# Optimization experiments

Hardware: AMD Instinct MI355X
Metric: run time of the kernel (lower is better)

The kernel has to match this reference:

```python
import jax, jax.numpy as jnp
import numpy as np

N_NODES = 50000
N_EDGES = 1600000
N_GRAPHS = 64
IN_DIM = 128
HID = 128
N_CLASSES = 10


def setup_inputs() -> dict:
    key = jax.random.key(0)
    ks = jax.random.split(key, 12)
    x = jax.random.normal(ks[0], (N_NODES, IN_DIM), dtype=jnp.float32)
    edge_index = jax.random.randint(ks[1], (2, N_EDGES), 0, N_NODES, dtype=jnp.int32)
    batch = jnp.sort(jax.random.randint(ks[2], (N_NODES,), 0, N_GRAPHS, dtype=jnp.int32))
    def glorot(k, shape):
        s = 1.0 / np.sqrt(shape[0])
        return jax.random.uniform(k, shape, jnp.float32, -s, s)
    W1 = glorot(ks[3], (IN_DIM, HID)); b1 = jnp.zeros((HID,), jnp.float32)
    W2 = glorot(ks[4], (HID, HID));    b2 = jnp.zeros((HID,), jnp.float32)
    Wc1 = glorot(ks[5], (HID, HID));   bc1 = glorot(ks[6], (HID,))
    Wc2 = glorot(ks[7], (HID, N_CLASSES)); bc2 = glorot(ks[8], (N_CLASSES,))
    return {"x": x, "edge_index": edge_index, "batch": batch,
            "W1": W1, "b1": b1, "W2": W2, "b2": b2,
            "Wc1": Wc1, "bc1": bc1, "Wc2": Wc2, "bc2": bc2}


def gcn_conv(x, edge_index, W, b):
    """PyG GCNConv: sym-normalized A-hat (with self loops) @ (x W) + b."""
    n = x.shape[0]
    loop = jnp.arange(n, dtype=edge_index.dtype)
    src = jnp.concatenate([edge_index[0], loop])  # message source
    dst = jnp.concatenate([edge_index[1], loop])  # message target
    deg = jax.ops.segment_sum(jnp.ones_like(src, dtype=x.dtype), dst, num_segments=n)
    dinv = jnp.where(deg > 0, jax.lax.rsqrt(deg), jnp.zeros_like(deg))
    norm = dinv[src] * dinv[dst]  # [E+N]
    h = x @ W                     # [N, H]
    msg = h[src] * norm[:, None]  # gather + scale
    out = jax.ops.segment_sum(msg, dst, num_segments=n)
    return out + b


def reference(x, edge_index, batch, W1, b1, W2, b2, Wc1, bc1, Wc2, bc2):
    h = jax.nn.relu(gcn_conv(x, edge_index, W1, b1))
    h = jax.nn.relu(gcn_conv(h, edge_index, W2, b2))
    # per-graph mean pooling (segment mean)
    sums = jax.ops.segment_sum(h, batch, num_segments=N_GRAPHS)
    cnt = jax.ops.segment_sum(jnp.ones((h.shape[0],), h.dtype), batch, num_segments=N_GRAPHS)
    g = sums / jnp.clip(cnt, 1.0)[:, None]  # [G, H]
    z = jax.nn.relu(g @ Wc1 + bc1)
    return z @ Wc2 + bc2
```

## Files before the change

### kernel.cpp

```cpp
#include <hip/hip_runtime.h>
#include <cstdint>
#include <cstddef>

#define CHUNK 4096

typedef __attribute__((ext_vector_type(8))) short short8;
typedef __attribute__((ext_vector_type(4))) float f32x4;
typedef __attribute__((ext_vector_type(2))) float f32x2;
typedef __attribute__((ext_vector_type(4))) unsigned int u32x4;

__device__ __forceinline__ float bf2f(unsigned short u) {
  return __uint_as_float(((unsigned)u) << 16);
}
__device__ __forceinline__ unsigned short f2bf(float f) {
  unsigned u = __float_as_uint(f);
  u += 0x7fffu + ((u >> 16) & 1u);
  return (unsigned short)(u >> 16);
}
__device__ __forceinline__ f32x2 unpk(unsigned u) {
  f32x2 r;
  r.x = __uint_as_float(u << 16);
  r.y = __uint_as_float(u & 0xffff0000u);
  return r;
}
__device__ __forceinline__ void pkfma(f32x2& a, f32x2 b, f32x2 c) {
  asm("v_pk_fma_f32 %0, %1, %2, %0" : "+v"(a) : "v"(b), "v"(c));
}

union SMem {
  unsigned short ws[128 * 136];
  struct { int c[256]; int cur[256]; int sb[256]; } cf;
};

__global__ void prep_k(const float* __restrict__ W1, const float* __restrict__ W2,
                       unsigned short* __restrict__ W1t, unsigned short* __restrict__ W2t,
                       int* __restrict__ gcur, int B) {
  int idx = blockIdx.x * 256 + threadIdx.x;
  const float* W = (idx < 16384) ? W1 : W2;
  unsigned short* Wt = (idx < 16384) ? W1t : W2t;
  int i = idx & 16383;
  int k = i >> 7, n = i & 127;
  Wt[n * 128 + k] = f2bf(W[i]);
  if (blockIdx.x == 0 && threadIdx.x < B) gcur[threadIdx.x] = 0;
}

__global__ __launch_bounds__(256) void scatter_atomic_k(const int* __restrict__ src,
                                                        const int* __restrict__ dst, int E,
                                                        int* __restrict__ gcur,
                                                        unsigned int* __restrict__ tmp,
                                                        int cap, int B) {
  __shared__ unsigned pk[CHUNK];
  __shared__ unsigned char bk[CHUNK];
  __shared__ int h[256];
  __shared__ int cur[256];
  __shared__ int base_s[256];
  int t = threadIdx.x;
  h[t] = 0;
  __syncthreads();
  int e0 = blockIdx.x * CHUNK;
  int e1 = e0 + CHUNK; if (e1 > E) e1 = E;
  int m = e1 - e0;
  for (int i = t; i < m; i += 256) {
    int d = dst[e0 + i], s = src[e0 + i];
    int b = d >> 8;
    pk[i] = ((unsigned)s << 8) | (unsigned)(d & 255);
    bk[i] = (unsigned char)b;
    atomicAdd(&h[b], 1);
  }
  __syncthreads();
  if (t < B && h[t] > 0) base_s[t] = atomicAdd(&gcur[t], h[t]);
  cur[t] = 0;
  __syncthreads();
  for (int i = t; i < m; i += 256) {
    int b = bk[i];
    int r = atomicAdd(&cur[b], 1);
    int p = base_s[b] + r;
    if (p < cap) tmp[(size_t)b * cap + p] = pk[i];
  }
}

template <bool AF32>
__device__ __forceinline__ void gemm_tile(SMem& sm, const void* Ap,
                                          const unsigned short* Wt,
                                          unsigned short* C, int N, int tile) {
  for (int idx = threadIdx.x; idx < 2048; idx += 256) {
    int n = idx >> 4, c = idx & 15;
    *(uint4*)&sm.ws[n * 136 + c * 8] = ((const uint4*)Wt)[idx];
  }
  __syncthreads();
  const int w = threadIdx.x >> 6;
  const int lane = threadIdx.x & 63;
  const int quad = lane >> 4, l16 = lane & 15;
  const int r = tile * 64 + w * 16 + l16;
  f32x4 acc[8] = {};
  #pragma unroll
  for (int ks = 0; ks < 4; ks++) {
    short8 a = {};
    if (r < N) {
      if (AF32) {
        const float* ar = (const float*)Ap + (size_t)r * 128 + ks * 32 + quad * 8;
        float4 u0 = *(const float4*)ar;
        float4 u1 = *(const float4*)(ar + 4);
        a[0] = (short)f2bf(u0.x); a[1] = (short)f2bf(u0.y);
        a[2] = (short)f2bf(u0.z); a[3] = (short)f2bf(u0.w);
        a[4] = (short)f2bf(u1.x); a[5] = (short)f2bf(u1.y);
        a[6] = (short)f2bf(u1.z); a[7] = (short)f2bf(u1.w);
      } else {
        a = *(const short8*)((const unsigned short*)Ap + (size_t)r * 128 + ks * 32 + quad * 8);
      }
    }
    #pragma unroll
    for (int t = 0; t < 8; t++) {
      short8 bF = *(const short8*)&sm.ws[(t * 16 + l16) * 136 + ks * 32 + quad * 8];
      acc[t] = __builtin_amdgcn_mfma_f32_16x16x32_bf16(a, bF, acc[t], 0, 0, 0);
    }
  }
  __syncthreads();
  unsigned short* Cs = sm.ws;
  {
    int rloc = w * 16 + quad * 4;
    #pragma unroll
    for (int t = 0; t < 8; t++)
      #pragma unroll
      for (int rg = 0; rg < 4; rg++)
        Cs[(rloc + rg) * 132 + t * 16 + l16] = f2bf(acc[t][rg]);
  }
  __syncthreads();
  const int r0 = tile * 64;
  for (int idx = threadIdx.x; idx < 1024; idx += 256) {
    int row = idx >> 4, c = idx & 15;
    int rr = r0 + row;
    if (rr < N) {
      uint2 a = *(uint2*)&Cs[row * 132 + c * 8];
      uint2 b = *(uint2*)&Cs[row * 132 + c * 8 + 4];
      ((uint4*)C)[(size_t)rr * 16 + c] = make_uint4(a.x, a.y, b.x, b.y);
    }
  }
}

__global__ __launch_bounds__(256) void cntfill_gemm1_k(const unsigned int* __restrict__ tmp,
                                                       const int* __restrict__ gcur,
                                                       int N, int E, int cap, int B,
                                                       float* __restrict__ dinv,
                                                       int* __restrict__ rs,
                                                       unsigned short* __restrict__ col,
                                                       const float* __restrict__ x,
                                                       const unsigned short* __restrict__ W1t,
                                                       unsigned short* __restrict__ B2) {
  __shared__ SMem sm;
  const int t = threadIdx.x;
  if ((int)blockIdx.x >= B) {
    gemm_tile<true>(sm, x, W1t, B2, N, blockIdx.x - B);
    return;
  }
  int b = blockIdx.x;
  int cb = 0;
  if (t < B) { cb = gcur[t]; if (cb > cap) cb = cap; }
  sm.cf.sb[t] = cb;
  __syncthreads();
  for (int off = 1; off < 256; off <<= 1) {
    int u = (t >= off) ? sm.cf.sb[t - off] : 0;
    __syncthreads();
    sm.cf.sb[t] += u;
    __syncthreads();
  }
  int base_b = (b > 0) ? sm.cf.sb[b - 1] : 0;
  int cnt_b = sm.cf.sb[b] - base_b;
  if (b == 0 && t == 0) rs[N] = sm.cf.sb[B - 1];
  const unsigned* tb = tmp + (size_t)b * cap;
  sm.cf.c[t] = 0;
  __syncthreads();
  for (int i = t; i < cnt_b; i += 256) atomicAdd(&sm.cf.c[tb[i] & 255u], 1);
  __syncthreads();
  int v = sm.cf.c[t];
  sm.cf.cur[t] = v;
  __syncthreads();
  for (int off = 1; off < 256; off <<= 1) {
    int u = (t >= off) ? sm.cf.cur[t - off] : 0;
    __syncthreads();
    sm.cf.cur[t] += u;
    __syncthreads();
  }
  int rsv = base_b + sm.cf.cur[t] - v;
  int node = (b << 8) + t;
  if (node < N) {
    rs[node] = rsv;
    dinv[node] = rsqrtf((float)v + 1.0f);
  }
  __syncthreads();
  sm.cf.cur[t] = rsv;
  __syncthreads();
  for (int i = t; i < cnt_b; i += 256) {
    unsigned u = tb[i];
    int pos = atomicAdd(&sm.cf.cur[u & 255u], 1);
    col[pos] = (unsigned short)(u >> 8);
  }
}

template <bool AF32>
__global__ __launch_bounds__(256) void gemm_bf_k(const void* __restrict__ Ap,
                                                 const unsigned short* __restrict__ Wt,
                                                 unsigned short* __restrict__ C, int N) {
  __shared__ SMem sm;
  gemm_tile<AF32>(sm, Ap, Wt, C, N, blockIdx.x);
}

template <typename CT>
__global__ __launch_bounds__(256) void agg32_k(const unsigned short* __restrict__ h,
                                               const int* __restrict__ rs,
                                               const CT* __restrict__ col,
                                               const float* __restrict__ dinv,
                                               const float* __restrict__ bias,
                                               unsigned short* __restrict__ outp, int n) {
  int wid = (blockIdx.x * blockDim.x + threadIdx.x) >> 6;
  int lane = threadIdx.x & 63;
  if (wid >= n) return;
  const int g = lane >> 4;
  const int l = lane & 15;
  float di = dinv[wid];
  f32x2 acc2[4];
  {
    uint4 sv = ((const uint4*)(h + (size_t)wid * 128))[l];
    float ws = (g == 0) ? di : 0.f;
    f32x2 wv; wv.x = ws; wv.y = ws;
    acc2[0] = unpk(sv.x) * wv;
    acc2[1] = unpk(sv.y) * wv;
    acc2[2] = unpk(sv.z) * wv;
    acc2[3] = unpk(sv.w) * wv;
  }
  int beg = rs[wid], end = rs[wid + 1];
  int base = beg;
  for (; base + 32 <= end; base += 32) {
    int s[8];
    float w[8];
    uint4 H[8];
    #pragma unroll
    for (int k = 0; k < 8; k++) s[k] = (int)col[base + 4 * k + g];
    #pragma unroll
    for (int k = 0; k < 8; k++) w[k] = dinv[s[k]];
    #pragma unroll
    for (int k = 0; k < 8; k++) H[k] = ((const uint4*)(h + (size_t)s[k] * 128))[l];
    #pragma unroll
    for (int k = 0; k < 8; k++) {
      f32x2 wv; wv.x = w[k]; wv.y = w[k];
      pkfma(acc2[0], unpk(H[k].x), wv);
      pkfma(acc2[1], unpk(H[k].y), wv);
      pkfma(acc2[2], unpk(H[k].z), wv);
      pkfma(acc2[3], unpk(H[k].w), wv);
    }
  }
  for (; base < end; base += 16) {
    int e0 = base + g, e1 = base + 4 + g, e2 = base + 8 + g, e3 = base + 12 + g;
    int i0 = (e0 < end) ? e0 : end - 1;
    int i1 = (e1 < end) ? e1 : end - 1;
    int i2 = (e2 < end) ? e2 : end - 1;
    int i3 = (e3 < end) ? e3 : end - 1;
    int s0 = (int)col[i0], s1 = (int)col[i1], s2 = (int)col[i2], s3 = (int)col[i3];
    float w0 = (e0 < end) ? dinv[s0] : 0.f;
    float w1 = (e1 < end) ? dinv[s1] : 0.f;
    float w2 = (e2 < end) ? dinv[s2] : 0.f;
    float w3 = (e3 < end) ? dinv[s3] : 0.f;
    uint4 h0 = ((const uint4*)(h + (size_t)s0 * 128))[l];
    uint4 h1 = ((const uint4*)(h + (size_t)s1 * 128))[l];
    uint4 h2 = ((const uint4*)(h + (size_t)s2 * 128))[l];
    uint4 h3 = ((const uint4*)(h + (size_t)s3 * 128))[l];
    f32x2 w0v; w0v.x = w0; w0v.y = w0;
    f32x2 w1v; w1v.x = w1; w1v.y = w1;
    f32x2 w2v; w2v.x = w2; w2v.y = w2;
    f32x2 w3v; w3v.x = w3; w3v.y = w3;
    pkfma(acc2[0], unpk(h0.x), w0v); pkfma(acc2[0], unpk(h1.x), w1v);
    pkfma(acc2[0], unpk(h2.x), w2v); pkfma(acc2[0], unpk(h3.x), w3v);
    pkfma(acc2[1], unpk(h0.y), w0v); pkfma(acc2[1], unpk(h1.y), w1v);
    pkfma(acc2[1], unpk(h2.y), w2v); pkfma(acc2[1], unpk(h3.y), w3v);
    pkfma(acc2[2], unpk(h0.z), w0v); pkfma(acc2[2], unpk(h1.z), w1v);
    pkfma(acc2[2], unpk(h2.z), w2v); pkfma(acc2[2], unpk(h3.z), w3v);
    pkfma(acc2[3], unpk(h0.w), w0v); pkfma(acc2[3], unpk(h1.w), w1v);
    pkfma(acc2[3], unpk(h2.w), w2v); pkfma(acc2[3], unpk(h3.w), w3v);
  }
  #pragma unroll
  for (int j = 0; j < 4; j++) {
    acc2[j].x += __shfl_xor(acc2[j].x, 16);
    acc2[j].y += __shfl_xor(acc2[j].y, 16);
    acc2[j].x += __shfl_xor(acc2[j].x, 32);
    acc2[j].y += __shfl_xor(acc2[j].y, 32);
  }
  if (g == 0) {
    float4 bA = *(const float4*)(bias + l * 8);
    float4 bB = *(const float4*)(bias + l * 8 + 4);
    float r0 = fmaxf(acc2[0].x * di + bA.x, 0.f);
    float r1 = fmaxf(acc2[0].y * di + bA.y, 0.f);
    float r2 = fmaxf(acc2[1].x * di + bA.z, 0.f);
    float r3 = fmaxf(acc2[1].y * di + bA.w, 0.f);
    float r4 = fmaxf(acc2[2].x * di + bB.x, 0.f);
    float r5 = fmaxf(acc2[2].y * di + bB.y, 0.f);
    float r6 = fmaxf(acc2[3].x * di + bB.z, 0.f);
    float r7 = fmaxf(acc2[3].y * di + bB.w, 0.f);
    u32x4 v;
    v.x = (unsigned)f2bf(r0) | ((unsigned)f2bf(r1) << 16);
    v.y = (unsigned)f2bf(r2) | ((unsigned)f2bf(r3) << 16);
    v.z = (unsigned)f2bf(r4) | ((unsigned)f2bf(r5) << 16);
    v.w = (unsigned)f2bf(r6) | ((unsigned)f2bf(r7) << 16);
    __builtin_nontemporal_store(v, (u32x4*)outp + (size_t)wid * 16 + l);
  }
}

__global__ __launch_bounds__(256) void poolclassify2_k(const unsigned short* __restrict__ h,
                                                       const int* __restrict__ bat, int n,
                                                       const float* __restrict__ Wc1,
                                                       const float* __restrict__ bc1,
                                                       const float* __restrict__ Wc2,
                                                       const float* __restrict__ bc2,
                                                       float* __restrict__ out, int nc) {
  __shared__ float red[16][136];
  __shared__ float gs[128];
  __shared__ float zs[128];
  const int g = blockIdx.x;
  const int t = threadIdx.x;
  const int slot = t >> 4;
  const int seg = t & 15;
  int lo;
  {
    int l = 0, r = n;
    while (l < r) { int m = (l + r) >> 1; if (bat[m] < g) l = m + 1; else r = m; }
    lo = l;
  }
  int hi;
  {
    int l = lo, r = n;
    while (l < r) { int m = (l + r) >> 1; if (bat[m] < g + 1) l = m + 1; else r = m; }
    hi = l;
  }
  float a0 = 0.f, a1 = 0.f, a2 = 0.f, a3 = 0.f, a4 = 0.f, a5 = 0.f, a6 = 0.f, a7 = 0.f;
  for (int i = lo + slot; i < hi; i += 16) {
    uint4 v = ((const uint4*)(h + (size_t)i * 128))[seg];
    a0 += bf2f((unsigned short)v.x);  a1 += bf2f((unsigned short)(v.x >> 16));
    a2 += bf2f((unsigned short)v.y);  a3 += bf2f((unsigned short)(v.y >> 16));
    a4 += bf2f((unsigned short)v.z);  a5 += bf2f((unsigned short)(v.z >> 16));
    a6 += bf2f((unsigned short)v.w);  a7 += bf2f((unsigned short)(v.w >> 16));
  }
  red[slot][seg * 8 + 0] = a0; red[slot][seg * 8 + 1] = a1;
  red[slot][seg * 8 + 2] = a2; red[slot][seg * 8 + 3] = a3;
  red[slot][seg * 8 + 4] = a4; red[slot][seg * 8 + 5] = a5;
  red[slot][seg * 8 + 6] = a6; red[slot][seg * 8 + 7] = a7;
  __syncthreads();
  if (t < 128) {
    float c = (float)(hi - lo); if (c < 1.f) c = 1.f;
    float s = 0.f;
    #pragma unroll
    for (int k = 0; k < 16; k++) s += red[k][t];
    gs[t] = s / c;
  }
  __syncthreads();
  if (t < 128) {
    float a = bc1[t];
    for (int k = 0; k < 128; k++) a += gs[k] * Wc1[k * 128 + t];
    zs[t] = fmaxf(a, 0.f);
  }
  __syncthreads();
  if (t < nc) {
    float o = bc2[t];
    for (int k = 0; k < 128; k++) o += zs[k] * Wc2[k * nc + t];
    out[g * nc + t] = o;
  }
}

__global__ void count_edges_k(const int* __restrict__ dst, int E, int* __restrict__ cnt) {
  int e = blockIdx.x * blockDim.x + threadIdx.x;
  if (e < E) atomicAdd(&cnt[dst[e]], 1);
}
__global__ void dinv_k(const int* __restrict__ cnt, float* __restrict__ dinv, int n) {
  int i = blockIdx.x * blockDim.x + threadIdx.x;
  if (i < n) dinv[i] = rsqrtf((float)cnt[i] + 1.0f);
}
__global__ void fill_csr_k(const int* __restrict__ src, const int* __restrict__ dst, int E,
                           int* __restrict__ cursor, int* __restrict__ col) {
  int e = blockIdx.x * blockDim.x + threadIdx.x;
  if (e < E) {
    int d = dst[e], s = src[e];
    int pos = atomicAdd(&cursor[d], 1);
    col[pos] = s;
  }
}
__global__ void scan1_k(const int* __restrict__ cnt, int* __restrict__ rs,
                        int* __restrict__ partials, int n) {
  __shared__ int s[1024];
  int t = threadIdx.x;
  int gid = blockIdx.x * 1024 + t;
  int v = (gid < n) ? cnt[gid] : 0;
  s[t] = v;
  __syncthreads();
  for (int off = 1; off < 1024; off <<= 1) {
    int u = (t >= off) ? s[t - off] : 0;
    __syncthreads();
    s[t] += u;
    __syncthreads();
  }
  if (gid < n) rs[gid] = s[t] - v;
  if (t == 1023) partials[blockIdx.x] = s[1023];
}
__global__ void scan2_k(int* __restrict__ partials, int nb) {
  if (threadIdx.x == 0 && blockIdx.x == 0) {
    int acc = 0;
    for (int i = 0; i < nb; i++) { int v = partials[i]; partials[i] = acc; acc += v; }
  }
}
__global__ void scan3_k(int* __restrict__ rs, int* __restrict__ cursor,
                        const int* __restrict__ partials, int n, int total) {
  int gid = blockIdx.x * blockDim.x + threadIdx.x;
  if (gid < n) {
    int v = rs[gid] + partials[gid >> 10];
    rs[gid] = v;
    cursor[gid] = v;
  }
  if (gid == 0) rs[n] = total;
}

extern "C" void kernel_launch(void* const* d_in, const int* in_sizes, int n_in,
                              void* d_out, int out_size, void* d_ws, size_t ws_size,
                              hipStream_t stream) {
  const float* x   = (const float*)d_in[0];
  const int*   ei  = (const int*)d_in[1];
  const int*   bat = (const int*)d_in[2];
  const float* W1  = (const float*)d_in[3];
  const float* b1  = (const float*)d_in[4];
  const float* W2  = (const float*)d_in[5];
  const float* b2  = (const float*)d_in[6];
  const float* Wc1 = (const float*)d_in[7];
  const float* bc1 = (const float*)d_in[8];
  const float* Wc2 = (const float*)d_in[9];
  const float* bc2 = (const float*)d_in[10];
  float* out = (float*)d_out;

  const int N  = in_sizes[0] / 128;
  const int E  = in_sizes[1] / 2;
  const int NC = in_sizes[10];
  const int G  = out_size / NC;
  const int* src = ei;
  const int* dst = ei + E;
  (void)n_in; (void)ws_size;

  size_t off = 0;
  auto walloc = [&](size_t bytes) -> void* {
    void* p = (char*)d_ws + off;
    off += (bytes + 255) & ~(size_t)255;
    return p;
  };
  unsigned short* B2 = (unsigned short*)walloc((size_t)N * 128 * 2);
  unsigned short* B3 = (unsigned short*)walloc((size_t)N * 128 * 2);
  unsigned short* W1t = (unsigned short*)walloc(128 * 128 * 2);
  unsigned short* W2t = (unsigned short*)walloc(128 * 128 * 2);
  float* dinv = (float*)walloc((size_t)N * 4);
  int*   rs   = (int*)  walloc((size_t)(N + 1) * 4);

  const bool small = (N <= 65535);
  const int gblocks = (N + 63) / 64;
  const int aggGrid = (N + 3) / 4;

  if (small) {
    const int B    = (N + 255) >> 8;
    const int nblk = (E + CHUNK - 1) / CHUNK;
    const int cap  = (E + B - 1) / B + 2048;
    unsigned short* col = (unsigned short*)walloc((size_t)E * 2);
    unsigned int*   tmp = (unsigned int*)  walloc((size_t)B * cap * 4);
    int* gcur = (int*)walloc((size_t)B * 4);

    prep_k<<<128, 256, 0, stream>>>(W1, W2, W1t, W2t, gcur, B);
    scatter_atomic_k<<<nblk, 256, 0, stream>>>(src, dst, E, gcur, tmp, cap, B);
    cntfill_gemm1_k<<<B + gblocks, 256, 0, stream>>>(tmp, gcur, N, E, cap, B,
                                                     dinv, rs, col, x, W1t, B2);
    agg32_k<unsigned short><<<aggGrid, 256, 0, stream>>>(B2, rs, col, dinv, b1, B3, N);
    gemm_bf_k<false><<<gblocks, 256, 0, stream>>>(B3, W2t, B2, N);
    agg32_k<unsigned short><<<aggGrid, 256, 0, stream>>>(B2, rs, col, dinv, b2, B3, N);
    poolclassify2_k<<<G, 256, 0, stream>>>(B3, bat, N, Wc1, bc1, Wc2, bc2, out, NC);
  } else {
    const int nb = (N + 1023) / 1024;
    int* cnt    = (int*)walloc((size_t)N * 4);
    int* cursor = (int*)walloc((size_t)N * 4);
    int* col    = (int*)walloc((size_t)E * 4);
    int* partials = (int*)walloc(256 * 4);
    prep_k<<<128, 256, 0, stream>>>(W1, W2, W1t, W2t, cnt , 0);
    (void)hipMemsetAsync(cnt, 0, (size_t)N * 4, stream);
    count_edges_k<<<(E + 255) / 256, 256, 0, stream>>>(dst, E, cnt);
    scan1_k<<<nb, 1024, 0, stream>>>(cnt, rs, partials, N);
    scan2_k<<<1, 64, 0, stream>>>(partials, nb);
    scan3_k<<<(N + 255) / 256, 256, 0, stream>>>(rs, cursor, partials, N, E);
    dinv_k<<<(N + 255) / 256, 256, 0, stream>>>(cnt, dinv, N);
    fill_csr_k<<<(E + 255) / 256, 256, 0, stream>>>(src, dst, E, cursor, col);

    gemm_bf_k<true><<<gblocks, 256, 0, stream>>>(x, W1t, B2, N);
    agg32_k<int><<<aggGrid, 256, 0, stream>>>(B2, rs, col, dinv, b1, B3, N);
    gemm_bf_k<false><<<gblocks, 256, 0, stream>>>(B3, W2t, B2, N);
    agg32_k<int><<<aggGrid, 256, 0, stream>>>(B2, rs, col, dinv, b2, B3, N);
    poolclassify2_k<<<G, 256, 0, stream>>>(B3, bat, N, Wc1, bc1, Wc2, bc2, out, NC);
  }
}
```

Baseline: 285.9 us.

## Fuse mean-pool into second aggregation, locally sort scatter, stage CSR fill in LDS

The second GCN aggregation now adds its ReLU outputs straight into per-graph sums with float atomics, so the hidden tensor is no longer written and re-read by the pooling kernel. A small classify kernel finishes the mean and the MLP. The edge scatter kernel now counting-sorts each chunk by bucket in shared memory before writing, which makes global writes contiguous. The CSR column fill is staged in LDS and then copied out coalesced. The cost is heavy atomic contention on 64 graph rows, a larger LDS union, and a float summation order that is no longer deterministic.

```diff
diff --git a/kernel.cpp b/kernel.cpp
--- a/kernel.cpp
+++ b/kernel.cpp
@@ -29,12 +29,14 @@
 
 union SMem {
   unsigned short ws[128 * 136];
-  struct { int c[256]; int cur[256]; int sb[256]; } cf;
+  struct { int c[256]; int cur[256]; int sb[256];
+           unsigned short colL[12288]; } cf;
 };
 
 __global__ void prep_k(const float* __restrict__ W1, const float* __restrict__ W2,
                        unsigned short* __restrict__ W1t, unsigned short* __restrict__ W2t,
-                       int* __restrict__ gcur, int B) {
+                       int* __restrict__ gcur, int B,
+                       float* __restrict__ gsums, int GN) {
   int idx = blockIdx.x * 256 + threadIdx.x;
   const float* W = (idx < 16384) ? W1 : W2;
   unsigned short* Wt = (idx < 16384) ? W1t : W2t;
@@ -42,18 +44,19 @@
   int k = i >> 7, n = i & 127;
   Wt[n * 128 + k] = f2bf(W[i]);
   if (blockIdx.x == 0 && threadIdx.x < B) gcur[threadIdx.x] = 0;
-}
-
-__global__ __launch_bounds__(256) void scatter_atomic_k(const int* __restrict__ src,
-                                                        const int* __restrict__ dst, int E,
-                                                        int* __restrict__ gcur,
-                                                        unsigned int* __restrict__ tmp,
-                                                        int cap, int B) {
-  __shared__ unsigned pk[CHUNK];
-  __shared__ unsigned char bk[CHUNK];
+  if (idx < GN) gsums[idx] = 0.f;
+}
+
+__global__ __launch_bounds__(256) void scatter_sort_k(const int* __restrict__ src,
+                                                      const int* __restrict__ dst, int E,
+                                                      int* __restrict__ gcur,
+                                                      unsigned int* __restrict__ tmp,
+                                                      int cap, int B) {
+  __shared__ unsigned sorted[CHUNK];
   __shared__ int h[256];
+  __shared__ int lps[256];
+  __shared__ int base_s[256];
   __shared__ int cur[256];
-  __shared__ int base_s[256];
   int t = threadIdx.x;
   h[t] = 0;
   __syncthreads();
@@ -61,21 +64,35 @@
   int e1 = e0 + CHUNK; if (e1 > E) e1 = E;
   int m = e1 - e0;
   for (int i = t; i < m; i += 256) {
+    atomicAdd(&h[dst[e0 + i] >> 8], 1);
+  }
+  __syncthreads();
+  int v = h[t];
+  lps[t] = v;
+  __syncthreads();
+  for (int off = 1; off < 256; off <<= 1) {
+    int u = (t >= off) ? lps[t - off] : 0;
+    __syncthreads();
+    lps[t] += u;
+    __syncthreads();
+  }
+  int incl = lps[t];
+  if (t < B && v > 0) base_s[t] = atomicAdd(&gcur[t], v);
+  cur[t] = 0;
+  lps[t] = incl - v;
+  __syncthreads();
+  for (int i = t; i < m; i += 256) {
     int d = dst[e0 + i], s = src[e0 + i];
     int b = d >> 8;
-    pk[i] = ((unsigned)s << 8) | (unsigned)(d & 255);
-    bk[i] = (unsigned char)b;
-    atomicAdd(&h[b], 1);
-  }
-  __syncthreads();
-  if (t < B && h[t] > 0) base_s[t] = atomicAdd(&gcur[t], h[t]);
-  cur[t] = 0;
+    int r = atomicAdd(&cur[b], 1);
+    sorted[lps[b] + r] = ((unsigned)b << 24) | ((unsigned)s << 8) | (unsigned)(d & 255);
+  }
   __syncthreads();
   for (int i = t; i < m; i += 256) {
-    int b = bk[i];
-    int r = atomicAdd(&cur[b], 1);
-    int p = base_s[b] + r;
-    if (p < cap) tmp[(size_t)b * cap + p] = pk[i];
+    unsigned u = sorted[i];
+    int b = u >> 24;
+    int p = base_s[b] + (i - lps[b]);
+    if (p < cap) tmp[(size_t)b * cap + p] = u;
   }
 }
 
@@ -188,12 +205,24 @@
     dinv[node] = rsqrtf((float)v + 1.0f);
   }
   __syncthreads();
-  sm.cf.cur[t] = rsv;
-  __syncthreads();
-  for (int i = t; i < cnt_b; i += 256) {
-    unsigned u = tb[i];
-    int pos = atomicAdd(&sm.cf.cur[u & 255u], 1);
-    col[pos] = (unsigned short)(u >> 8);
+  if (cnt_b <= 12288) {
+    sm.cf.cur[t] = rsv - base_b;
+    __syncthreads();
+    for (int i = t; i < cnt_b; i += 256) {
+      unsigned u = tb[i];
+      int lpos = atomicAdd(&sm.cf.cur[u & 255u], 1);
+      sm.cf.colL[lpos] = (unsigned short)((u >> 8) & 0xFFFFu);
+    }
+    __syncthreads();
+    for (int i = t; i < cnt_b; i += 256) col[base_b + i] = sm.cf.colL[i];
+  } else {
+    sm.cf.cur[t] = rsv;
+    __syncthreads();
+    for (int i = t; i < cnt_b; i += 256) {
+      unsigned u = tb[i];
+      int pos = atomicAdd(&sm.cf.cur[u & 255u], 1);
+      col[pos] = (unsigned short)((u >> 8) & 0xFFFFu);
+    }
   }
 }
 
@@ -206,29 +235,11 @@
 }
 
 template <typename CT>
-__global__ __launch_bounds__(256) void agg32_k(const unsigned short* __restrict__ h,
-                                               const int* __restrict__ rs,
-                                               const CT* __restrict__ col,
-                                               const float* __restrict__ dinv,
-                                               const float* __restrict__ bias,
-                                               unsigned short* __restrict__ outp, int n) {
-  int wid = (blockIdx.x * blockDim.x + threadIdx.x) >> 6;
-  int lane = threadIdx.x & 63;
-  if (wid >= n) return;
-  const int g = lane >> 4;
-  const int l = lane & 15;
-  float di = dinv[wid];
-  f32x2 acc2[4];
-  {
-    uint4 sv = ((const uint4*)(h + (size_t)wid * 128))[l];
-    float ws = (g == 0) ? di : 0.f;
-    f32x2 wv; wv.x = ws; wv.y = ws;
-    acc2[0] = unpk(sv.x) * wv;
-    acc2[1] = unpk(sv.y) * wv;
-    acc2[2] = unpk(sv.z) * wv;
-    acc2[3] = unpk(sv.w) * wv;
-  }
-  int beg = rs[wid], end = rs[wid + 1];
+__device__ __forceinline__ void agg_body(f32x2 (&acc2)[4],
+                                         const unsigned short* __restrict__ h,
+                                         const CT* __restrict__ col,
+                                         const float* __restrict__ dinv,
+                                         int beg, int end, int g, int l) {
   int base = beg;
   for (; base + 32 <= end; base += 32) {
     int s[8];
@@ -284,6 +295,32 @@
     acc2[j].x += __shfl_xor(acc2[j].x, 32);
     acc2[j].y += __shfl_xor(acc2[j].y, 32);
   }
+}
+
+template <typename CT>
+__global__ __launch_bounds__(256) void agg32_k(const unsigned short* __restrict__ h,
+                                               const int* __restrict__ rs,
+                                               const CT* __restrict__ col,
+                                               const float* __restrict__ dinv,
+                                               const float* __restrict__ bias,
+                                               unsigned short* __restrict__ outp, int n) {
+  int wid = (blockIdx.x * blockDim.x + threadIdx.x) >> 6;
+  int lane = threadIdx.x & 63;
+  if (wid >= n) return;
+  const int g = lane >> 4;
+  const int l = lane & 15;
+  float di = dinv[wid];
+  f32x2 acc2[4];
+  {
+    uint4 sv = ((const uint4*)(h + (size_t)wid * 128))[l];
+    float ws = (g == 0) ? di : 0.f;
+    f32x2 wv; wv.x = ws; wv.y = ws;
+    acc2[0] = unpk(sv.x) * wv;
+    acc2[1] = unpk(sv.y) * wv;
+    acc2[2] = unpk(sv.z) * wv;
+    acc2[3] = unpk(sv.w) * wv;
+  }
+  agg_body<CT>(acc2, h, col, dinv, rs[wid], rs[wid + 1], g, l);
   if (g == 0) {
     float4 bA = *(const float4*)(bias + l * 8);
     float4 bB = *(const float4*)(bias + l * 8 + 4);
@@ -301,6 +338,95 @@
     v.z = (unsigned)f2bf(r4) | ((unsigned)f2bf(r5) << 16);
     v.w = (unsigned)f2bf(r6) | ((unsigned)f2bf(r7) << 16);
     __builtin_nontemporal_store(v, (u32x4*)outp + (size_t)wid * 16 + l);
+  }
+}
+
+template <typename CT>
+__global__ __launch_bounds__(256) void aggpool_k(const unsigned short* __restrict__ h,
+                                                 const int* __restrict__ rs,
+                                                 const CT* __restrict__ col,
+                                                 const float* __restrict__ dinv,
+                                                 const float* __restrict__ bias,
+                                                 const int* __restrict__ bat,
+                                                 float* __restrict__ gsums, int n) {
+  int wid = (blockIdx.x * blockDim.x + threadIdx.x) >> 6;
+  int lane = threadIdx.x & 63;
+  if (wid >= n) return;
+  const int g = lane >> 4;
+  const int l = lane & 15;
+  float di = dinv[wid];
+  f32x2 acc2[4];
+  {
+    uint4 sv = ((const uint4*)(h + (size_t)wid * 128))[l];
+    float ws = (g == 0) ? di : 0.f;
+    f32x2 wv; wv.x = ws; wv.y = ws;
+    acc2[0] = unpk(sv.x) * wv;
+    acc2[1] = unpk(sv.y) * wv;
+    acc2[2] = unpk(sv.z) * wv;
+    acc2[3] = unpk(sv.w) * wv;
+  }
+  agg_body<CT>(acc2, h, col, dinv, rs[wid], rs[wid + 1], g, l);
+  if (g == 0) {
+    float4 bA = *(const float4*)(bias + l * 8);
+    float4 bB = *(const float4*)(bias + l * 8 + 4);
+    float r0 = fmaxf(acc2[0].x * di + bA.x, 0.f);
+    float r1 = fmaxf(acc2[0].y * di + bA.y, 0.f);
+    float r2 = fmaxf(acc2[1].x * di + bA.z, 0.f);
+    float r3 = fmaxf(acc2[1].y * di + bA.w, 0.f);
+    float r4 = fmaxf(acc2[2].x * di + bB.x, 0.f);
+    float r5 = fmaxf(acc2[2].y * di + bB.y, 0.f);
+    float r6 = fmaxf(acc2[3].x * di + bB.z, 0.f);
+    float r7 = fmaxf(acc2[3].y * di + bB.w, 0.f);
+    float* gp = gsums + (size_t)bat[wid] * 128 + l * 8;
+    unsafeAtomicAdd(gp + 0, r0);
+    unsafeAtomicAdd(gp + 1, r1);
+    unsafeAtomicAdd(gp + 2, r2);
+    unsafeAtomicAdd(gp + 3, r3);
+    unsafeAtomicAdd(gp + 4, r4);
+    unsafeAtomicAdd(gp + 5, r5);
+    unsafeAtomicAdd(gp + 6, r6);
+    unsafeAtomicAdd(gp + 7, r7);
+  }
+}
+
+__global__ __launch_bounds__(256) void classify_k(const float* __restrict__ gsums,
+                                                  const int* __restrict__ bat, int n,
+                                                  const float* __restrict__ Wc1,
+                                                  const float* __restrict__ bc1,
+                                                  const float* __restrict__ Wc2,
+                                                  const float* __restrict__ bc2,
+                                                  float* __restrict__ out, int nc) {
+  __shared__ float gs[128];
+  __shared__ float zs[128];
+  const int g = blockIdx.x;
+  const int t = threadIdx.x;
+  int lo;
+  {
+    int l = 0, r = n;
+    while (l < r) { int m = (l + r) >> 1; if (bat[m] < g) l = m + 1; else r = m; }
+    lo = l;
+  }
+  int hi;
+  {
+    int l = lo, r = n;
+    while (l < r) { int m = (l + r) >> 1; if (bat[m] < g + 1) l = m + 1; else r = m; }
+    hi = l;
+  }
+  if (t < 128) {
+    float c = (float)(hi - lo); if (c < 1.f) c = 1.f;
+    gs[t] = gsums[g * 128 + t] / c;
+  }
+  __syncthreads();
+  if (t < 128) {
+    float a = bc1[t];
+    for (int k = 0; k < 128; k++) a += gs[k] * Wc1[k * 128 + t];
+    zs[t] = fmaxf(a, 0.f);
+  }
+  __syncthreads();
+  if (t < nc) {
+    float o = bc2[t];
+    for (int k = 0; k < 128; k++) o += zs[k] * Wc2[k * nc + t];
+    out[g * nc + t] = o;
   }
 }
 
@@ -451,6 +577,7 @@
   unsigned short* W2t = (unsigned short*)walloc(128 * 128 * 2);
   float* dinv = (float*)walloc((size_t)N * 4);
   int*   rs   = (int*)  walloc((size_t)(N + 1) * 4);
+  float* gsums = (float*)walloc((size_t)G * 128 * 4);
 
   const bool small = (N <= 65535);
   const int gblocks = (N + 63) / 64;
@@ -464,21 +591,21 @@
     unsigned int*   tmp = (unsigned int*)  walloc((size_t)B * cap * 4);
     int* gcur = (int*)walloc((size_t)B * 4);
 
-    prep_k<<<128, 256, 0, stream>>>(W1, W2, W1t, W2t, gcur, B);
-    scatter_atomic_k<<<nblk, 256, 0, stream>>>(src, dst, E, gcur, tmp, cap, B);
+    prep_k<<<128, 256, 0, stream>>>(W1, W2, W1t, W2t, gcur, B, gsums, G * 128);
+    scatter_sort_k<<<nblk, 256, 0, stream>>>(src, dst, E, gcur, tmp, cap, B);
     cntfill_gemm1_k<<<B + gblocks, 256, 0, stream>>>(tmp, gcur, N, E, cap, B,
                                                      dinv, rs, col, x, W1t, B2);
     agg32_k<unsigned short><<<aggGrid, 256, 0, stream>>>(B2, rs, col, dinv, b1, B3, N);
     gemm_bf_k<false><<<gblocks, 256, 0, stream>>>(B3, W2t, B2, N);
-    agg32_k<unsigned short><<<aggGrid, 256, 0, stream>>>(B2, rs, col, dinv, b2, B3, N);
-    poolclassify2_k<<<G, 256, 0, stream>>>(B3, bat, N, Wc1, bc1, Wc2, bc2, out, NC);
+    aggpool_k<unsigned short><<<aggGrid, 256, 0, stream>>>(B2, rs, col, dinv, b2, bat, gsums, N);
+    classify_k<<<G, 256, 0, stream>>>(gsums, bat, N, Wc1, bc1, Wc2, bc2, out, NC);
   } else {
     const int nb = (N + 1023) / 1024;
     int* cnt    = (int*)walloc((size_t)N * 4);
     int* cursor = (int*)walloc((size_t)N * 4);
     int* col    = (int*)walloc((size_t)E * 4);
     int* partials = (int*)walloc(256 * 4);
-    prep_k<<<128, 256, 0, stream>>>(W1, W2, W1t, W2t, cnt , 0);
+    prep_k<<<128, 256, 0, stream>>>(W1, W2, W1t, W2t, cnt , 0, gsums, G * 128);
     (void)hipMemsetAsync(cnt, 0, (size_t)N * 4, stream);
     count_edges_k<<<(E + 255) / 256, 256, 0, stream>>>(dst, E, cnt);
     scan1_k<<<nb, 1024, 0, stream>>>(cnt, rs, partials, N);
```

New measurement: 771.4 us. 2.7x slower.
